# Kernel tuning notes

Hardware: AMD Instinct MI355X
Metric: run time of the kernel (lower is better)

## Reference

```python
import jax, jax.numpy as jnp
import numpy as np

D_MODEL = 1024
D_STATE = 16
EXPAND = 2
D_INNER = D_MODEL * EXPAND
DT_RANK = D_MODEL // 16


def setup_inputs() -> dict:
    key = jax.random.key(0)
    ks = jax.random.split(key, 12)
    B, T = 2, 2048
    s_in = 1.0 / np.sqrt(D_MODEL)
    s_x = 1.0 / np.sqrt(D_INNER)
    s_dt = 1.0 / np.sqrt(DT_RANK)
    inp = {
        'u': jax.random.normal(ks[0], (B, T, D_MODEL), jnp.float32),
        'W_in': jax.random.uniform(ks[1], (2 * D_INNER, D_MODEL), jnp.float32, -s_in, s_in),
        'b_in': jax.random.uniform(ks[2], (2 * D_INNER,), jnp.float32, -s_in, s_in),
        'W_x': jax.random.uniform(ks[3], (DT_RANK + 2 * D_STATE, D_INNER), jnp.float32, -s_x, s_x),
        'b_x': jax.random.uniform(ks[4], (DT_RANK + 2 * D_STATE,), jnp.float32, -s_x, s_x),
        'W_dt': jax.random.uniform(ks[5], (D_INNER, DT_RANK), jnp.float32, -s_dt, s_dt),
        'b_dt': jax.random.uniform(ks[6], (D_INNER,), jnp.float32, -s_dt, s_dt),
        'A_log': jnp.log(jnp.abs(jax.random.normal(ks[7], (D_INNER, D_STATE), jnp.float32)) + 1e-6),
        'D': jnp.ones((D_INNER,), jnp.float32),
        'W_out': jax.random.uniform(ks[8], (D_MODEL, D_INNER), jnp.float32, -s_x, s_x),
        'b_out': jax.random.uniform(ks[9], (D_MODEL,), jnp.float32, -s_x, s_x),
    }
    return inp


def _ssm_forward(u, W_in, b_in, W_x, b_x, W_dt, b_dt, A_log, D, W_out, b_out):
    B, T, _ = u.shape
    u_inner = u @ W_in.T + b_in                       # [B,T,2*d_inner]
    x, z = jnp.split(u_inner, 2, axis=-1)             # each [B,T,d_inner]
    dbc = x @ W_x.T + b_x                             # [B,T,dt_rank+2N]
    delta_raw = dbc[..., :DT_RANK]
    B_ssm = dbc[..., DT_RANK:DT_RANK + D_STATE]       # [B,T,N]
    C_ssm = dbc[..., DT_RANK + D_STATE:]              # [B,T,N]
    delta = jax.nn.softplus(delta_raw @ W_dt.T + b_dt)  # [B,T,d_inner]
    A = -jnp.exp(A_log)                               # [d_inner,N]

    def step(h, xs):
        dt_t, x_t, Bt, Ct = xs                        # [B,d], [B,d], [B,N], [B,N]
        dA = jnp.exp(dt_t[..., None] * A)             # [B,d,N]
        dB = dt_t[..., None] * Bt[:, None, :]         # [B,d,N]
        h = h * dA + x_t[..., None] * dB
        y_t = jnp.einsum('bdn,bn->bd', h, Ct)
        return h, y_t

    h0 = jnp.zeros((B, D_INNER, D_STATE), u.dtype)
    xs = (jnp.swapaxes(delta, 0, 1), jnp.swapaxes(x, 0, 1),
          jnp.swapaxes(B_ssm, 0, 1), jnp.swapaxes(C_ssm, 0, 1))
    _, y = jax.lax.scan(step, h0, xs)                 # y: [T,B,d_inner]
    y = jnp.swapaxes(y, 0, 1)                         # [B,T,d_inner]
    y = y + x * D
    y = y * (z * jax.nn.sigmoid(z))                   # SiLU gate
    return y @ W_out.T + b_out                        # [B,T,d_model]


def reference(u, W_in, b_in, W_x, b_x, W_dt, b_dt, A_log, D, W_out, b_out):
    return _ssm_forward(u, W_in, b_in, W_x, b_x, W_dt, b_dt, A_log, D, W_out, b_out)
```

## Files before the change

### kernel.cpp

```cpp
#include <hip/hip_runtime.h>
#include <math.h>

#define BATCH 2
#define SEQ   2048
#define DM    1024
#define DI    2048
#define NST   16
#define MT    (BATCH*SEQ)
#define CHK   64
#define LCH   (SEQ/CHK)

typedef __attribute__((ext_vector_type(8))) short  bf16x8;
typedef __attribute__((ext_vector_type(4))) float  f32x4;

static __device__ __forceinline__ unsigned short f2bf(float f) {
  unsigned u = __float_as_uint(f);
  u += 0x7fff + ((u >> 16) & 1);
  return (unsigned short)(u >> 16);
}
static __device__ __forceinline__ float bf2f(unsigned short h) {
  return __uint_as_float(((unsigned)h) << 16);
}
static __device__ __forceinline__ float fexp2(float x) {
  float r;
  asm("v_exp_f32 %0, %1" : "=v"(r) : "v"(x));
  return r;
}
static __device__ __forceinline__ float flog2(float x) {
  float r;
  asm("v_log_f32 %0, %1" : "=v"(r) : "v"(x));
  return r;
}

#define SEG_U    (MT*DM/4)
#define SEG_WIN  (2*DI*DM/4)
#define SEG_WOUT (DM*DI/4)
#define SEG_WX   (96*DI/4)
#define SEG_WDT  (DI*64/4)
#define SEG_A    (DI*NST/4)
#define CUM0 SEG_U
#define CUM1 (CUM0+SEG_WIN)
#define CUM2 (CUM1+SEG_WOUT)
#define CUM3 (CUM2+SEG_WX)
#define CUM4 (CUM3+SEG_WDT)
#define CUM5 (CUM4+SEG_A)

__global__ __launch_bounds__(256) void convall_kernel(
    const float* __restrict__ u, const float* __restrict__ W_in,
    const float* __restrict__ W_out, const float* __restrict__ W_x,
    const float* __restrict__ W_dt, const float* __restrict__ A_log,
    unsigned short* __restrict__ u_bf, unsigned short* __restrict__ win_bf,
    unsigned short* __restrict__ wout_bf, unsigned short* __restrict__ wx_bf,
    unsigned short* __restrict__ wdt_bf, float* __restrict__ A2tab)
{
  const int gid = blockIdx.x*256 + threadIdx.x;
  const float4* src; ushort4* dst; int idx;
  if (gid < CUM0)      { idx = gid;        src = (const float4*)u;     dst = (ushort4*)u_bf; }
  else if (gid < CUM1) { idx = gid - CUM0; src = (const float4*)W_in;  dst = (ushort4*)win_bf; }
  else if (gid < CUM2) { idx = gid - CUM1; src = (const float4*)W_out; dst = (ushort4*)wout_bf; }
  else if (gid < CUM3) { idx = gid - CUM2; src = (const float4*)W_x;   dst = (ushort4*)wx_bf; }
  else if (gid < CUM4) { idx = gid - CUM3; src = (const float4*)W_dt;  dst = (ushort4*)wdt_bf; }
  else if (gid < CUM5) {
    int i = gid - CUM4;
    float4 v = ((const float4*)A_log)[i];
    float4 o;
    o.x = -1.44269504f * __expf(v.x);
    o.y = -1.44269504f * __expf(v.y);
    o.z = -1.44269504f * __expf(v.z);
    o.w = -1.44269504f * __expf(v.w);
    ((float4*)A2tab)[i] = o;
    return;
  } else return;
  float4 v = src[idx];
  ushort4 o;
  o.x = f2bf(v.x); o.y = f2bf(v.y); o.z = f2bf(v.z); o.w = f2bf(v.w);
  dst[idx] = o;
}

template<int BN, int BK, bool OUT_BF16, int LDC, int ACT>
__global__ __launch_bounds__(256, 4) void gemm2_kernel(
    const unsigned short* __restrict__ A,
    const unsigned short* __restrict__ B,
    const float* __restrict__ bias,
    void* __restrict__ Cout, int K, int nbx)
{
  constexpr int NH = BK / 32;
  constexpr int NJ = BN / 32;
  __shared__ unsigned short Abuf[2][NH][128*32];
  __shared__ unsigned short Bbuf[2][NH][BN*32];

  const int nwg = gridDim.x;
  const int cpx = nwg >> 3;
  const int bid = blockIdx.x;
  const int swz = (bid & 7) * cpx + (bid >> 3);
  const int bx = swz % nbx;
  const int by = swz / nbx;

  const int tid  = threadIdx.x;
  const int lane = tid & 63;
  const int wid  = tid >> 6;
  const int wr   = wid >> 1;
  const int wc   = wid & 1;
  const int lr    = lane >> 2;
  const int lslot = lane & 3;

  f32x4 zero = {0.f, 0.f, 0.f, 0.f};
  f32x4 acc[4][NJ];
#pragma unroll
  for (int i = 0; i < 4; ++i)
#pragma unroll
    for (int j = 0; j < NJ; ++j) acc[i][j] = zero;

  const size_t arow0 = (size_t)by * 128;
  const size_t brow0 = (size_t)bx * BN;
  const int NT = K / BK;

  auto STAGE = [&](int buf, int k0) {
#pragma unroll
    for (int half = 0; half < NH; ++half) {
#pragma unroll
      for (int i = 0; i < 2; ++i) {
        const int Rb = (wid + i*4) * 16;
        const int r  = Rb + lr;
        const int c8 = lslot ^ ((r >> 1) & 3);
        const unsigned short* ga = A + (arow0 + r)*(size_t)K + k0 + half*32 + c8*8;
        __builtin_amdgcn_global_load_lds(
            (const __attribute__((address_space(1))) void*)ga,
            (__attribute__((address_space(3))) void*)(&Abuf[buf][half][Rb*32]),
            16, 0, 0);
      }
#pragma unroll
      for (int i = 0; i < BN/64; ++i) {
        const int Rb = (wid + i*4) * 16;
        const int r  = Rb + lr;
        const int c8 = lslot ^ ((r >> 1) & 3);
        const unsigned short* gb = B + (brow0 + r)*(size_t)K + k0 + half*32 + c8*8;
        __builtin_amdgcn_global_load_lds(
            (const __attribute__((address_space(1))) void*)gb,
            (__attribute__((address_space(3))) void*)(&Bbuf[buf][half][Rb*32]),
            16, 0, 0);
      }
    }
  };

  STAGE(0, 0);
  __syncthreads();

  const int lrow = lane & 15, k8 = lane >> 4;
  int cur = 0;
  for (int kt = 0; kt < NT; ++kt) {
    if (kt + 1 < NT) STAGE(cur ^ 1, (kt + 1) * BK);

#pragma unroll
    for (int half = 0; half < NH; ++half) {
      bf16x8 af[4], bfr[NJ];
#pragma unroll
      for (int mi = 0; mi < 4; ++mi) {
        const int r = wr*64 + mi*16 + lrow;
        af[mi] = *(const bf16x8*)&Abuf[cur][half][r*32 + (k8 ^ ((r >> 1) & 3))*8];
      }
#pragma unroll
      for (int nj = 0; nj < NJ; ++nj) {
        const int r = wc*(BN/2) + nj*16 + lrow;
        bfr[nj] = *(const bf16x8*)&Bbuf[cur][half][r*32 + (k8 ^ ((r >> 1) & 3))*8];
      }
      __builtin_amdgcn_s_setprio(1);
#pragma unroll
      for (int mi = 0; mi < 4; ++mi)
#pragma unroll
        for (int nj = 0; nj < NJ; ++nj)
          acc[mi][nj] = __builtin_amdgcn_mfma_f32_16x16x32_bf16(
                            af[mi], bfr[nj], acc[mi][nj], 0, 0, 0);
      __builtin_amdgcn_s_setprio(0);
    }
    __syncthreads();
    cur ^= 1;
  }

  const int lcol = lane & 15, lrq = lane >> 4;
#pragma unroll
  for (int nj = 0; nj < NJ; ++nj) {
    const int colg = bx*BN + wc*(BN/2) + nj*16 + lcol;
    const float bv = bias[colg];
#pragma unroll
    for (int mi = 0; mi < 4; ++mi) {
      const int rowg = by*128 + wr*64 + mi*16 + lrq*4;
#pragma unroll
      for (int q = 0; q < 4; ++q) {
        float v = acc[mi][nj][q] + bv;
        if constexpr (ACT == 1) {
          float e = fexp2(-1.44269504f * fabsf(v));
          v = fmaxf(v, 0.f) + 0.69314718f * flog2(1.f + e);
        }
        if constexpr (OUT_BF16)
          ((unsigned short*)Cout)[(size_t)(rowg + q)*LDC + colg] = f2bf(v);
        else
          ((float*)Cout)[(size_t)(rowg + q)*LDC + colg] = v;
      }
    }
  }
}

__global__ __launch_bounds__(256) void dbc_mfma_kernel(
    const unsigned short* __restrict__ A,
    const unsigned short* __restrict__ Bw,
    float* __restrict__ partial)
{
  __shared__ unsigned short Abuf[64*32];
  __shared__ unsigned short Bbuf[96*32];

  const int tid  = threadIdx.x;
  const int lane = tid & 63;
  const int wid  = tid >> 6;
  const int lr    = lane >> 2;
  const int lslot = lane & 3;
  const size_t arow0 = (size_t)blockIdx.x * 64;
  const int ks   = blockIdx.y;
  const int k0b  = ks * (DI/4);

  f32x4 zero = {0.f, 0.f, 0.f, 0.f};
  f32x4 acc[6];
#pragma unroll
  for (int j = 0; j < 6; ++j) acc[j] = zero;

  for (int k0 = k0b; k0 < k0b + DI/4; k0 += 32) {
    {
      const int Rb = wid*16;
      const int r  = Rb + lr;
      const int c8 = lslot ^ ((r >> 1) & 3);
      const unsigned short* ga = A + (arow0 + r)*4096 + k0 + c8*8;
      __builtin_amdgcn_global_load_lds(
          (const __attribute__((address_space(1))) void*)ga,
          (__attribute__((address_space(3))) void*)(Abuf + Rb*32), 16, 0, 0);
    }
    if (wid < 3) {
#pragma unroll
      for (int i = 0; i < 2; ++i) {
        const int Rb = wid*32 + i*16;
        const int r  = Rb + lr;
        const int c8 = lslot ^ ((r >> 1) & 3);
        const unsigned short* gb = Bw + (size_t)r*DI + k0 + c8*8;
        __builtin_amdgcn_global_load_lds(
            (const __attribute__((address_space(1))) void*)gb,
            (__attribute__((address_space(3))) void*)(Bbuf + Rb*32), 16, 0, 0);
      }
    }
    __syncthreads();

    const int lrow = lane & 15, k8 = lane >> 4;
    const int ra = wid*16 + lrow;
    bf16x8 af = *(const bf16x8*)&Abuf[ra*32 + (k8 ^ ((ra >> 1) & 3))*8];
#pragma unroll
    for (int nj = 0; nj < 6; ++nj) {
      const int rb = nj*16 + lrow;
      bf16x8 bf_ = *(const bf16x8*)&Bbuf[rb*32 + (k8 ^ ((rb >> 1) & 3))*8];
      acc[nj] = __builtin_amdgcn_mfma_f32_16x16x32_bf16(af, bf_, acc[nj], 0, 0, 0);
    }
    __syncthreads();
  }

  const int lcol = lane & 15, lrq = lane >> 4;
  const int rowg = (int)arow0 + wid*16 + lrq*4;
#pragma unroll
  for (int nj = 0; nj < 6; ++nj) {
    const int colg = nj*16 + lcol;
#pragma unroll
    for (int q = 0; q < 4; ++q)
      partial[((size_t)ks*MT + rowg + q)*96 + colg] = acc[nj][q];
  }
}

__global__ __launch_bounds__(256) void dbc_reduce_kernel(
    const float* __restrict__ partial, const float* __restrict__ bx,
    float* __restrict__ dbc, unsigned short* __restrict__ draw_bf)
{
  const int gid = blockIdx.x*256 + threadIdx.x;
  const int m = gid / 96;
  const int c = gid - m*96;
  const size_t stride = (size_t)MT*96;
  float s = partial[gid] + partial[gid + stride]
          + partial[gid + 2*stride] + partial[gid + 3*stride] + bx[c];
  if (c < 64) draw_bf[(size_t)m*64 + c] = f2bf(s);
  else        dbc[(size_t)m*96 + c] = s;
}

__global__ __launch_bounds__(256) void scanA_kernel(
    const unsigned short* __restrict__ uib,
    const float* __restrict__ dbc,
    const unsigned short* __restrict__ delta_bf,
    const float* __restrict__ A2tab,
    float* __restrict__ P,
    float* __restrict__ S)
{
  const int bid = blockIdx.x;
  const int d   = (bid & 7)*256 + threadIdx.x;
  const int c   = (bid >> 3) & (CHK-1);
  const int b   = bid >> 9;

  float A2[NST];
  {
    const float4* ap = (const float4*)(A2tab + (size_t)d*NST);
#pragma unroll
    for (int q = 0; q < 4; ++q) {
      float4 v = ap[q];
      A2[q*4+0] = v.x; A2[q*4+1] = v.y; A2[q*4+2] = v.z; A2[q*4+3] = v.w;
    }
  }

  float h[NST];
#pragma unroll
  for (int nn = 0; nn < NST; ++nn) h[nn] = 0.f;
  float sdt = 0.f;

  const int t0 = c * LCH;
  const unsigned short* dptr = delta_bf + ((size_t)b*SEQ + t0)*DI + d;
  const unsigned short* xptr = uib      + ((size_t)b*SEQ + t0)*4096 + d;
  const float* bptr          = dbc      + ((size_t)b*SEQ + t0)*96 + 64;

  float dt = bf2f(dptr[0]);
  float xv = bf2f(xptr[0]);
  float4 Bv0 = *(const float4*)(bptr + 0);
  float4 Bv1 = *(const float4*)(bptr + 4);
  float4 Bv2 = *(const float4*)(bptr + 8);
  float4 Bv3 = *(const float4*)(bptr + 12);

  for (int t = 0; t < LCH; ++t) {
    const float dtc = dt, xvc = xv;
    float Bc[NST] = {Bv0.x,Bv0.y,Bv0.z,Bv0.w, Bv1.x,Bv1.y,Bv1.z,Bv1.w,
                     Bv2.x,Bv2.y,Bv2.z,Bv2.w, Bv3.x,Bv3.y,Bv3.z,Bv3.w};
    if (t + 1 < LCH) {
      const size_t tn = (size_t)(t+1);
      dt = bf2f(dptr[tn*DI]);
      xv = bf2f(xptr[tn*4096]);
      const float* bp = bptr + tn*96;
      Bv0 = *(const float4*)(bp + 0);
      Bv1 = *(const float4*)(bp + 4);
      Bv2 = *(const float4*)(bp + 8);
      Bv3 = *(const float4*)(bp + 12);
    }
    sdt += dtc;
    const float xdt = xvc * dtc;
#pragma unroll
    for (int nn = 0; nn < NST; ++nn) {
      float dA = fexp2(dtc * A2[nn]);
      h[nn] = h[nn]*dA + xdt*Bc[nn];
    }
  }

  float* Pp = P + (((size_t)b*CHK + c)*DI + d)*NST;
  float* Sp = S + (((size_t)b*CHK + c)*DI + d)*NST;
#pragma unroll
  for (int q = 0; q < 4; ++q) {
    float4 pv = { fexp2(A2[q*4+0]*sdt), fexp2(A2[q*4+1]*sdt),
                  fexp2(A2[q*4+2]*sdt), fexp2(A2[q*4+3]*sdt) };
    float4 sv = { h[q*4+0], h[q*4+1], h[q*4+2], h[q*4+3] };
    *(float4*)(Pp + q*4) = pv;
    *(float4*)(Sp + q*4) = sv;
  }
}

__global__ __launch_bounds__(256) void scanB_kernel(
    const float* __restrict__ P, float* __restrict__ S)
{
  const int gid = blockIdx.x*256 + threadIdx.x;
  const int n4 = gid & 3;
  const int d  = (gid >> 2) & (DI-1);
  const int b  = gid >> 13;

  float4 h = {0.f, 0.f, 0.f, 0.f};
  for (int c = 0; c < CHK; ++c) {
    const size_t idx = (((size_t)b*CHK + c)*DI + d)*NST + n4*4;
    float4 p = *(const float4*)(P + idx);
    float4 s = *(const float4*)(S + idx);
    *(float4*)(S + idx) = h;
    h.x = h.x*p.x + s.x;
    h.y = h.y*p.y + s.y;
    h.z = h.z*p.z + s.z;
    h.w = h.w*p.w + s.w;
  }
}

__global__ __launch_bounds__(256) void scanC_kernel(
    const unsigned short* __restrict__ uib,
    const float* __restrict__ dbc,
    const unsigned short* __restrict__ delta_bf,
    const float* __restrict__ A2tab,
    const float* __restrict__ Dp,
    const float* __restrict__ S,
    unsigned short* __restrict__ y_bf)
{
  const int bid = blockIdx.x;
  const int d   = (bid & 7)*256 + threadIdx.x;
  const int c   = (bid >> 3) & (CHK-1);
  const int b   = bid >> 9;

  float A2[NST];
  {
    const float4* ap = (const float4*)(A2tab + (size_t)d*NST);
#pragma unroll
    for (int q = 0; q < 4; ++q) {
      float4 v = ap[q];
      A2[q*4+0] = v.x; A2[q*4+1] = v.y; A2[q*4+2] = v.z; A2[q*4+3] = v.w;
    }
  }
  const float Dv = Dp[d];

  float h[NST];
  {
    const float* Sp = S + (((size_t)b*CHK + c)*DI + d)*NST;
#pragma unroll
    for (int q = 0; q < 4; ++q) {
      float4 sv = *(const float4*)(Sp + q*4);
      h[q*4+0] = sv.x; h[q*4+1] = sv.y; h[q*4+2] = sv.z; h[q*4+3] = sv.w;
    }
  }

  const int t0 = c * LCH;
  const unsigned short* dptr = delta_bf + ((size_t)b*SEQ + t0)*DI + d;
  const unsigned short* xptr = uib      + ((size_t)b*SEQ + t0)*4096 + d;
  const float* cptr          = dbc      + ((size_t)b*SEQ + t0)*96;
  unsigned short* yp         = y_bf     + ((size_t)b*SEQ + t0)*DI + d;

  float dt = bf2f(dptr[0]);
  float xv = bf2f(xptr[0]);
  float zv = bf2f(xptr[2048]);
  float4 Bv0 = *(const float4*)(cptr + 64);
  float4 Bv1 = *(const float4*)(cptr + 68);
  float4 Bv2 = *(const float4*)(cptr + 72);
  float4 Bv3 = *(const float4*)(cptr + 76);
  float4 Cv0 = *(const float4*)(cptr + 80);
  float4 Cv1 = *(const float4*)(cptr + 84);
  float4 Cv2 = *(const float4*)(cptr + 88);
  float4 Cv3 = *(const float4*)(cptr + 92);

  for (int t = 0; t < LCH; ++t) {
    const float dtc = dt, xvc = xv, zvc = zv;
    float Bc[NST] = {Bv0.x,Bv0.y,Bv0.z,Bv0.w, Bv1.x,Bv1.y,Bv1.z,Bv1.w,
                     Bv2.x,Bv2.y,Bv2.z,Bv2.w, Bv3.x,Bv3.y,Bv3.z,Bv3.w};
    float Cc[NST] = {Cv0.x,Cv0.y,Cv0.z,Cv0.w, Cv1.x,Cv1.y,Cv1.z,Cv1.w,
                     Cv2.x,Cv2.y,Cv2.z,Cv2.w, Cv3.x,Cv3.y,Cv3.z,Cv3.w};
    if (t + 1 < LCH) {
      const size_t tn = (size_t)(t+1);
      dt = bf2f(dptr[tn*DI]);
      xv = bf2f(xptr[tn*4096]);
      zv = bf2f(xptr[tn*4096 + 2048]);
      const float* cp = cptr + tn*96;
      Bv0 = *(const float4*)(cp + 64);
      Bv1 = *(const float4*)(cp + 68);
      Bv2 = *(const float4*)(cp + 72);
      Bv3 = *(const float4*)(cp + 76);
      Cv0 = *(const float4*)(cp + 80);
      Cv1 = *(const float4*)(cp + 84);
      Cv2 = *(const float4*)(cp + 88);
      Cv3 = *(const float4*)(cp + 92);
    }
    const float xdt = xvc * dtc;
    float y = 0.f;
#pragma unroll
    for (int nn = 0; nn < NST; ++nn) {
      float dA = fexp2(dtc * A2[nn]);
      h[nn] = h[nn]*dA + xdt*Bc[nn];
      y += h[nn]*Cc[nn];
    }
    y += xvc * Dv;
    y *= zvc / (1.f + fexp2(-1.44269504f * zvc));
    yp[(size_t)t*DI] = f2bf(y);
  }
}

extern "C" void kernel_launch(void* const* d_in, const int* in_sizes, int n_in,
                              void* d_out, int out_size, void* d_ws, size_t ws_size,
                              hipStream_t stream)
{
  const float* u     = (const float*)d_in[0];
  const float* W_in  = (const float*)d_in[1];
  const float* b_in  = (const float*)d_in[2];
  const float* W_x   = (const float*)d_in[3];
  const float* b_x   = (const float*)d_in[4];
  const float* W_dt  = (const float*)d_in[5];
  const float* b_dt  = (const float*)d_in[6];
  const float* A_log = (const float*)d_in[7];
  const float* Dp    = (const float*)d_in[8];
  const float* W_out = (const float*)d_in[9];
  const float* b_out = (const float*)d_in[10];
  float* out = (float*)d_out;

  unsigned short* ui_bf    = (unsigned short*)d_ws;
  float*          dbc      = (float*)(ui_bf + (size_t)MT*4096);
  unsigned short* delta_bf = (unsigned short*)(dbc + (size_t)MT*96);
  unsigned short* y_bf     = delta_bf + (size_t)MT*DI;
  unsigned short* wout_bf  = y_bf + (size_t)MT*DI;
  unsigned short* wx_bf    = wout_bf + (size_t)DM*DI;
  unsigned short* wdt_bf   = wx_bf + (size_t)96*DI;
  unsigned short* draw_bf  = wdt_bf + (size_t)DI*64;
  float*          S        = (float*)(draw_bf + (size_t)MT*64);
  float*          A2tab    = S + (size_t)BATCH*CHK*DI*NST;
  float*          partial  = A2tab + (size_t)DI*NST;

  unsigned short* u_bf   = (unsigned short*)d_out;
  unsigned short* win_bf = u_bf + (size_t)MT*DM;
  float* P = (float*)d_out;

  convall_kernel<<<CUM5/256, 256, 0, stream>>>(
      u, W_in, W_out, W_x, W_dt, A_log,
      u_bf, win_bf, wout_bf, wx_bf, wdt_bf, A2tab);

  gemm2_kernel<128, 32, true, 4096, 0><<<32*32, 256, 0, stream>>>(
      u_bf, win_bf, b_in, ui_bf, DM, 32);

  dbc_mfma_kernel<<<dim3(MT/64, 4), 256, 0, stream>>>(ui_bf, wx_bf, partial);
  dbc_reduce_kernel<<<MT*96/256, 256, 0, stream>>>(partial, b_x, dbc, draw_bf);

  gemm2_kernel<128, 32, true, 2048, 1><<<16*32, 256, 0, stream>>>(
      draw_bf, wdt_bf, b_dt, delta_bf, 64, 16);

  scanA_kernel<<<BATCH*CHK*DI/256, 256, 0, stream>>>(ui_bf, dbc, delta_bf, A2tab, P, S);
  scanB_kernel<<<BATCH*DI*4/256, 256, 0, stream>>>(P, S);
  scanC_kernel<<<BATCH*CHK*DI/256, 256, 0, stream>>>(ui_bf, dbc, delta_bf, A2tab, Dp, S, y_bf);

  gemm2_kernel<64, 64, false, 1024, 0><<<16*32, 256, 0, stream>>>(
      y_bf, wout_bf, b_out, out, DI, 16);
}
```

Measured before the change: 185.2 us.

## Add 256x256-tile 4-stage pipelined GEMM for input projection

Replaces the input-projection GEMM with a new kernel using 256x256 output tiles, 512 threads, and a 4-slot LDS ring filled by direct global-to-LDS loads with XOR swizzle. MFMA work is interleaved with staged A/B loads across barriers and uses setprio. The goal is more reuse per tile and better latency hiding on the largest GEMM. It needs 128KB of dynamic LDS, which allows only one block per CU, and falls back to the old kernel if the attribute cannot be set.

```diff
diff --git a/kernel.cpp b/kernel.cpp
--- a/kernel.cpp
+++ b/kernel.cpp
@@ -77,6 +77,154 @@
   dst[idx] = o;
 }
 
+#define MEMFENCE asm volatile("" ::: "memory")
+
+template<int K>
+__global__ __launch_bounds__(512, 2) void gemm3_kernel(
+    const unsigned short* __restrict__ A,
+    const unsigned short* __restrict__ B,
+    const float* __restrict__ bias,
+    unsigned short* __restrict__ Cout, int nbx)
+{
+  extern __shared__ unsigned short smem[];
+  unsigned short* As = smem;
+  unsigned short* Bs = smem + 4*256*32;
+  constexpr int NT = K / 32;
+
+  const int nwg = gridDim.x;
+  const int cpx = nwg >> 3;
+  const int bid = blockIdx.x;
+  const int swz = (bid & 7) * cpx + (bid >> 3);
+  const int bx = swz % nbx;
+  const int by = swz / nbx;
+
+  const int tid  = threadIdx.x;
+  const int lane = tid & 63;
+  const int wid  = tid >> 6;
+  const int wr   = wid >> 2;
+  const int wc   = wid & 3;
+
+  const size_t arow0 = (size_t)by * 256;
+  const size_t brow0 = (size_t)bx * 256;
+
+  const int s_r4 = lane >> 2;
+  const int s_c  = lane & 3;
+
+  auto STAGE_A = [&](int slot, int T) {
+#pragma unroll
+    for (int i = 0; i < 2; ++i) {
+      const int r  = wid*32 + i*16 + s_r4;
+      const int lc = s_c ^ (r & 3);
+      const unsigned short* g = A + (arow0 + r)*(size_t)K + T*32 + lc*8;
+      __builtin_amdgcn_global_load_lds(
+          (const __attribute__((address_space(1))) void*)g,
+          (__attribute__((address_space(3))) void*)(As + slot*(256*32) + (wid*32 + i*16)*32),
+          16, 0, 0);
+    }
+  };
+  auto STAGE_B = [&](int slot, int T) {
+#pragma unroll
+    for (int i = 0; i < 2; ++i) {
+      const int r  = wid*32 + i*16 + s_r4;
+      const int lc = s_c ^ (r & 3);
+      const unsigned short* g = B + (brow0 + r)*(size_t)K + T*32 + lc*8;
+      __builtin_amdgcn_global_load_lds(
+          (const __attribute__((address_space(1))) void*)g,
+          (__attribute__((address_space(3))) void*)(Bs + slot*(256*32) + (wid*32 + i*16)*32),
+          16, 0, 0);
+    }
+  };
+
+  f32x4 zero = {0.f, 0.f, 0.f, 0.f};
+  f32x4 acc[8][4];
+#pragma unroll
+  for (int i = 0; i < 8; ++i)
+#pragma unroll
+    for (int j = 0; j < 4; ++j) acc[i][j] = zero;
+
+  STAGE_A(0, 0); STAGE_B(0, 0);
+  STAGE_A(1, 1); STAGE_B(1, 1);
+  STAGE_A(2, 2); STAGE_B(2, 2);
+  asm volatile("s_waitcnt vmcnt(8)" ::: "memory");
+  __builtin_amdgcn_s_barrier();
+  MEMFENCE;
+
+  const int lrow = lane & 15, k8 = lane >> 4;
+  bf16x8 bfr[4];
+
+  for (int t = 0; t < NT; ++t) {
+    const int slot = t & 3;
+    const int sts  = (t + 3) & 3;
+    const unsigned short* Asl = As + slot*(256*32);
+    const unsigned short* Bsl = Bs + slot*(256*32);
+
+    bf16x8 af[4];
+#pragma unroll
+    for (int nj = 0; nj < 4; ++nj) {
+      const int r = wc*64 + nj*16 + lrow;
+      bfr[nj] = *(const bf16x8*)&Bsl[r*32 + (k8 ^ (r & 3))*8];
+    }
+#pragma unroll
+    for (int mi = 0; mi < 4; ++mi) {
+      const int r = wr*128 + mi*16 + lrow;
+      af[mi] = *(const bf16x8*)&Asl[r*32 + (k8 ^ (r & 3))*8];
+    }
+    if (t + 3 < NT) STAGE_A(sts, t + 3);
+    MEMFENCE;
+    __builtin_amdgcn_s_barrier();
+    MEMFENCE;
+    __builtin_amdgcn_s_setprio(1);
+#pragma unroll
+    for (int mi = 0; mi < 4; ++mi)
+#pragma unroll
+      for (int nj = 0; nj < 4; ++nj)
+        acc[mi][nj] = __builtin_amdgcn_mfma_f32_16x16x32_bf16(
+                          af[mi], bfr[nj], acc[mi][nj], 0, 0, 0);
+    __builtin_amdgcn_s_setprio(0);
+    MEMFENCE;
+    __builtin_amdgcn_s_barrier();
+    MEMFENCE;
+
+#pragma unroll
+    for (int mi = 0; mi < 4; ++mi) {
+      const int r = wr*128 + 64 + mi*16 + lrow;
+      af[mi] = *(const bf16x8*)&Asl[r*32 + (k8 ^ (r & 3))*8];
+    }
+    if (t + 3 < NT) STAGE_B(sts, t + 3);
+    MEMFENCE;
+    __builtin_amdgcn_s_barrier();
+    MEMFENCE;
+    __builtin_amdgcn_s_setprio(1);
+#pragma unroll
+    for (int mi = 0; mi < 4; ++mi)
+#pragma unroll
+      for (int nj = 0; nj < 4; ++nj)
+        acc[mi + 4][nj] = __builtin_amdgcn_mfma_f32_16x16x32_bf16(
+                              af[mi], bfr[nj], acc[mi + 4][nj], 0, 0, 0);
+    __builtin_amdgcn_s_setprio(0);
+
+    if (t <= NT - 4)      asm volatile("s_waitcnt vmcnt(8)" ::: "memory");
+    else if (t == NT - 3) asm volatile("s_waitcnt vmcnt(4)" ::: "memory");
+    else                  asm volatile("s_waitcnt vmcnt(0)" ::: "memory");
+    __builtin_amdgcn_s_barrier();
+    MEMFENCE;
+  }
+
+  const int lcol = lane & 15, lrq = lane >> 4;
+#pragma unroll
+  for (int nj = 0; nj < 4; ++nj) {
+    const int colg = bx*256 + wc*64 + nj*16 + lcol;
+    const float bv = bias[colg];
+#pragma unroll
+    for (int mi = 0; mi < 8; ++mi) {
+      const int rowg = by*256 + wr*128 + mi*16 + lrq*4;
+#pragma unroll
+      for (int q = 0; q < 4; ++q)
+        Cout[(size_t)(rowg + q)*4096 + colg] = f2bf(acc[mi][nj][q] + bv);
+    }
+  }
+}
+
 template<int BN, int BK, bool OUT_BF16, int LDC, int ACT>
 __global__ __launch_bounds__(256, 4) void gemm2_kernel(
     const unsigned short* __restrict__ A,
@@ -505,8 +653,16 @@
       u, W_in, W_out, W_x, W_dt, A_log,
       u_bf, win_bf, wout_bf, wx_bf, wdt_bf, A2tab);
 
-  gemm2_kernel<128, 32, true, 4096, 0><<<32*32, 256, 0, stream>>>(
-      u_bf, win_bf, b_in, ui_bf, DM, 32);
+  bool big = hipFuncSetAttribute(
+      (const void*)gemm3_kernel<DM>,
+      hipFuncAttributeMaxDynamicSharedMemorySize, 131072) == hipSuccess;
+  if (big) {
+    gemm3_kernel<DM><<<16*16, 512, 131072, stream>>>(
+        u_bf, win_bf, b_in, ui_bf, 16);
+  } else {
+    gemm2_kernel<128, 32, true, 4096, 0><<<32*32, 256, 0, stream>>>(
+        u_bf, win_bf, b_in, ui_bf, DM, 32);
+  }
 
   dbc_mfma_kernel<<<dim3(MT/64, 4), 256, 0, stream>>>(ui_bf, wx_bf, partial);
   dbc_reduce_kernel<<<MT*96/256, 256, 0, stream>>>(partial, b_x, dbc, draw_bf);
```

Result: no change. 187.4 us (+1.2%).
